# Kernel optimization log

Hardware: AMD Instinct MI355X
Metric: run time of the kernel (lower is better)

The kernel has to match this reference:

```python
import jax, jax.numpy as jnp
import numpy as np


def soft_threshold(x, theta):
    # sign(x) * relu(|x| - theta)
    return jnp.sign(x) * jax.nn.relu(jnp.abs(x) - theta)


def setup_inputs() -> dict:
    key = jax.random.key(0)
    k1, k2, k3, k4 = jax.random.split(key, 4)
    B, n, m = 16384, 256, 1024
    X = jax.random.normal(k1, (B, n), dtype=jnp.float32)
    # xavier-like scaling for weights
    We = jax.random.normal(k2, (m, n), dtype=jnp.float32) * (1.0 / np.sqrt(n))
    S = jax.random.normal(k3, (m, m), dtype=jnp.float32) * (1.0 / np.sqrt(m))
    theta = jax.random.uniform(k4, (m,), dtype=jnp.float32) * 0.1 + 0.05
    return {"X": X, "We": We, "S": S, "theta": theta}


def reference(X, We, S, theta):
    T = 16  # number of unrolled LISTA steps
    B = X @ We.T                      # (batch, m)
    Z0 = soft_threshold(B, theta)

    def step(Z, _):
        C = B + Z @ S.T               # (batch, m)
        Z_new = soft_threshold(C, theta)
        return Z_new, None

    Z, _ = jax.lax.scan(step, Z0, None, length=T)
    return Z
```

## Files before the change

kernel.cpp:

```cpp
#include <hip/hip_runtime.h>
#include <hip/hip_bf16.h>
#include <cstdint>


typedef __attribute__((ext_vector_type(8))) short short8;
typedef __attribute__((ext_vector_type(4))) float floatx4;

__device__ __forceinline__ void g2lds16(const void* g, void* lds) {
    __builtin_amdgcn_global_load_lds(
        (const __attribute__((address_space(1))) uint32_t*)(uintptr_t)g,
        (__attribute__((address_space(3))) uint32_t*)(uintptr_t)lds,
        16, 0, 0);
}

template<int KSTEPS, bool FIRST, bool LAST>
__global__ void __launch_bounds__(256, 3)
lista_gemm(const unsigned short* __restrict__ A,
           const unsigned short* __restrict__ W,
           const float* __restrict__ Bmat_in,
           float* __restrict__ Bmat_out,
           const float* __restrict__ theta,
           unsigned short* __restrict__ Zout,
           float* __restrict__ Fout)
{
    constexpr int K  = KSTEPS * 64;
    constexpr int N  = 1024;
    constexpr int KB = K * 2;

    __shared__ unsigned short Ash[128 * 64];
    __shared__ unsigned short Bsh[128 * 64];

    const int t    = threadIdx.x;
    const int bm   = blockIdx.x;
    const int bn   = blockIdx.y;
    const int wave = t >> 6;
    const int lane = t & 63;
    const int wm   = wave >> 1;
    const int wn   = wave & 1;

    floatx4 acc[4][4];
#pragma unroll
    for (int i = 0; i < 4; ++i)
#pragma unroll
        for (int j = 0; j < 4; ++j) acc[i][j] = (floatx4){0.f, 0.f, 0.f, 0.f};

    const int r0 = t >> 3;
    const int ch = t & 7;

    const char* Abase = (const char*)A + (size_t)(bm * 128) * KB;
    const char* Wbase = (const char*)W + (size_t)(bn * 128) * KB;

    for (int kt = 0; kt < KSTEPS; ++kt) {
        __syncthreads();
#pragma unroll
        for (int c = 0; c < 4; ++c) {
            const int r = r0 + c * 32;
            const int g = ch ^ (r & 7);
            const size_t goff = (size_t)r * KB + (size_t)kt * 128 + g * 16;
            const int loff = (c * 256 + t) * 16;
            g2lds16(Abase + goff, (char*)Ash + loff);
            g2lds16(Wbase + goff, (char*)Bsh + loff);
        }
        __syncthreads();

#pragma unroll
        for (int kk = 0; kk < 2; ++kk) {
            short8 af[4], bf[4];
            const int q  = lane >> 4;
            const int rl = lane & 15;
            const int gq = kk * 4 + q;
#pragma unroll
            for (int mi = 0; mi < 4; ++mi) {
                const int R = wm * 64 + mi * 16 + rl;
                af[mi] = *(const short8*)((const char*)Ash + R * 128 + ((gq ^ (R & 7)) * 16));
            }
#pragma unroll
            for (int ni = 0; ni < 4; ++ni) {
                const int R = wn * 64 + ni * 16 + rl;
                bf[ni] = *(const short8*)((const char*)Bsh + R * 128 + ((gq ^ (R & 7)) * 16));
            }
#pragma unroll
            for (int mi = 0; mi < 4; ++mi)
#pragma unroll
                for (int ni = 0; ni < 4; ++ni)
                    acc[mi][ni] = __builtin_amdgcn_mfma_f32_16x16x32_bf16(
                        af[mi], bf[ni], acc[mi][ni], 0, 0, 0);
        }
    }

    const int col_base = bn * 128 + wn * 64;
    const int row_base = bm * 128 + wm * 64;
#pragma unroll
    for (int ni = 0; ni < 4; ++ni) {
        const int col = col_base + ni * 16 + (lane & 15);
        const float th = theta[col];
#pragma unroll
        for (int mi = 0; mi < 4; ++mi) {
            const int row0 = row_base + mi * 16 + (lane >> 4) * 4;
#pragma unroll
            for (int v = 0; v < 4; ++v) {
                const size_t idx = (size_t)(row0 + v) * N + col;
                float c = acc[mi][ni][v];
                if constexpr (!FIRST) c += Bmat_in[idx];
                if constexpr (FIRST)  Bmat_out[idx] = c;
                const float a = fabsf(c) - th;
                const float z = a > 0.f ? (c > 0.f ? a : -a) : 0.f;
                if constexpr (LAST) {
                    Fout[idx] = z;
                } else {
                    __hip_bfloat16 hb = __float2bfloat16(z);
                    Zout[idx] = *(unsigned short*)&hb;
                }
            }
        }
    }
}

__global__ void __launch_bounds__(256)
cvt4(const float* __restrict__ s, unsigned short* __restrict__ d, int n4)
{
    const int i = blockIdx.x * blockDim.x + threadIdx.x;
    if (i < n4) {
        const float4 v = ((const float4*)s)[i];
        ushort4 o;
        __hip_bfloat16 b;
        b = __float2bfloat16(v.x); o.x = *(unsigned short*)&b;
        b = __float2bfloat16(v.y); o.y = *(unsigned short*)&b;
        b = __float2bfloat16(v.z); o.z = *(unsigned short*)&b;
        b = __float2bfloat16(v.w); o.w = *(unsigned short*)&b;
        ((ushort4*)d)[i] = o;
    }
}

extern "C" void kernel_launch(void* const* d_in, const int* in_sizes, int n_in,
                              void* d_out, int out_size, void* d_ws, size_t ws_size,
                              hipStream_t stream) {
    const float* X     = (const float*)d_in[0];
    const float* We    = (const float*)d_in[1];
    const float* S     = (const float*)d_in[2];
    const float* theta = (const float*)d_in[3];
    float* out = (float*)d_out;

    char* ws = (char*)d_ws;
    unsigned short* S_bf  = (unsigned short*)(ws);
    unsigned short* X_bf  = (unsigned short*)(ws + (size_t)(2)   * 1048576);
    unsigned short* We_bf = (unsigned short*)(ws + (size_t)(10)  * 1048576);
    float*          Bmat  = (float*)         (ws + (size_t)(11)  * 1048576);
    unsigned short* Za    = (unsigned short*)(ws + (size_t)(75)  * 1048576);
    unsigned short* Zb    = (unsigned short*)(ws + (size_t)(107) * 1048576);

    cvt4<<<dim3(1024), dim3(256), 0, stream>>>(S,  S_bf,  1024 * 1024 / 4);
    cvt4<<<dim3(4096), dim3(256), 0, stream>>>(X,  X_bf,  16384 * 256 / 4);
    cvt4<<<dim3(256),  dim3(256), 0, stream>>>(We, We_bf, 1024 * 256 / 4);

    const dim3 grid(128, 8), blk(256);

    lista_gemm<4, true, false><<<grid, blk, 0, stream>>>(
        X_bf, We_bf, nullptr, Bmat, theta, Za, nullptr);

    unsigned short* zin = Za;
    unsigned short* zout = Zb;
    for (int tstep = 1; tstep <= 15; ++tstep) {
        lista_gemm<16, false, false><<<grid, blk, 0, stream>>>(
            zin, S_bf, Bmat, nullptr, theta, zout, nullptr);
        unsigned short* tmp = zin; zin = zout; zout = tmp;
    }
    lista_gemm<16, false, true><<<grid, blk, 0, stream>>>(
        zin, S_bf, Bmat, nullptr, theta, nullptr, out);
}
```

Measured before the change: 1.048 ms.

## Fuse all LISTA steps into one persistent kernel with Z resident in LDS

Replaces the 17 separate GEMM launches with one kernel in which each 512-thread block owns 64 batch rows. The block keeps its Z tile (64x1024 bf16, 128KB) in swizzled LDS across all 16 steps and keeps B in registers, packed as bf16. This removes the global round-trips of Z and the fp32 B matrix, plus the launch overhead. In exchange, S is streamed directly from global/L2 into registers with no LDS staging. Only 256 blocks run, and B is now stored in bf16 precision, which adds rounding error.

```diff
diff --git a/kernel.cpp b/kernel.cpp
--- a/kernel.cpp
+++ b/kernel.cpp
@@ -6,110 +6,159 @@
 typedef __attribute__((ext_vector_type(8))) short short8;
 typedef __attribute__((ext_vector_type(4))) float floatx4;
 
-__device__ __forceinline__ void g2lds16(const void* g, void* lds) {
-    __builtin_amdgcn_global_load_lds(
-        (const __attribute__((address_space(1))) uint32_t*)(uintptr_t)g,
-        (__attribute__((address_space(3))) uint32_t*)(uintptr_t)lds,
-        16, 0, 0);
+__device__ __forceinline__ unsigned short f2b(float f) {
+    __hip_bfloat16 h = __float2bfloat16(f);
+    return *(unsigned short*)&h;
+}
+__device__ __forceinline__ float b2f(unsigned short u) {
+    union { unsigned int i; float f; } x; x.i = ((unsigned int)u) << 16; return x.f;
 }
 
-template<int KSTEPS, bool FIRST, bool LAST>
-__global__ void __launch_bounds__(256, 3)
-lista_gemm(const unsigned short* __restrict__ A,
-           const unsigned short* __restrict__ W,
-           const float* __restrict__ Bmat_in,
-           float* __restrict__ Bmat_out,
-           const float* __restrict__ theta,
-           unsigned short* __restrict__ Zout,
-           float* __restrict__ Fout)
+__global__ void __launch_bounds__(512, 2)
+lista_fused(const unsigned short* __restrict__ Xbf,
+            const unsigned short* __restrict__ Webf,
+            const unsigned short* __restrict__ Sbf,
+            const float* __restrict__ theta,
+            float* __restrict__ out)
 {
-    constexpr int K  = KSTEPS * 64;
-    constexpr int N  = 1024;
-    constexpr int KB = K * 2;
-
-    __shared__ unsigned short Ash[128 * 64];
-    __shared__ unsigned short Bsh[128 * 64];
+    __shared__ __align__(16) unsigned short Zd[64 * 1024];
 
     const int t    = threadIdx.x;
-    const int bm   = blockIdx.x;
-    const int bn   = blockIdx.y;
     const int wave = t >> 6;
     const int lane = t & 63;
-    const int wm   = wave >> 1;
-    const int wn   = wave & 1;
+    const int l15  = lane & 15;
+    const int q    = lane >> 4;
+    const int blk  = blockIdx.x;
 
-    floatx4 acc[4][4];
+    floatx4 acc[4][8];
+    unsigned int Bpk[4][8][2];
+
+    const char* Sb = (const char*)Sbf  + ((size_t)(wave * 128 + l15) * 1024 + q * 8) * 2;
+    const char* Xb = (const char*)Xbf  + ((size_t)(blk * 64   + l15) * 256  + q * 8) * 2;
+    const char* Wb = (const char*)Webf + ((size_t)(wave * 128 + l15) * 256  + q * 8) * 2;
+
 #pragma unroll
-    for (int i = 0; i < 4; ++i)
+    for (int mi = 0; mi < 4; ++mi)
 #pragma unroll
-        for (int j = 0; j < 4; ++j) acc[i][j] = (floatx4){0.f, 0.f, 0.f, 0.f};
+        for (int ni = 0; ni < 8; ++ni) acc[mi][ni] = (floatx4){0.f, 0.f, 0.f, 0.f};
 
-    const int r0 = t >> 3;
-    const int ch = t & 7;
+#pragma unroll
+    for (int kc = 0; kc < 8; ++kc) {
+        short8 af[4];
+#pragma unroll
+        for (int mi = 0; mi < 4; ++mi)
+            af[mi] = *(const short8*)(Xb + mi * 8192 + kc * 64);
+#pragma unroll
+        for (int h = 0; h < 2; ++h) {
+            short8 sf[4];
+#pragma unroll
+            for (int j = 0; j < 4; ++j)
+                sf[j] = *(const short8*)(Wb + (h * 4 + j) * 8192 + kc * 64);
+#pragma unroll
+            for (int mi = 0; mi < 4; ++mi)
+#pragma unroll
+                for (int j = 0; j < 4; ++j)
+                    acc[mi][h * 4 + j] = __builtin_amdgcn_mfma_f32_16x16x32_bf16(
+                        af[mi], sf[j], acc[mi][h * 4 + j], 0, 0, 0);
+        }
+    }
 
-    const char* Abase = (const char*)A + (size_t)(bm * 128) * KB;
-    const char* Wbase = (const char*)W + (size_t)(bn * 128) * KB;
+#pragma unroll
+    for (int mi = 0; mi < 4; ++mi) {
+#pragma unroll
+        for (int ni = 0; ni < 8; ++ni) {
+            const int col   = wave * 128 + ni * 16 + l15;
+            const float th  = theta[col];
+            const int chunk = col >> 3;
+            const int coff  = (col & 7) * 2;
+#pragma unroll
+            for (int vp = 0; vp < 2; ++vp) {
+                const float c0 = acc[mi][ni][vp * 2 + 0];
+                const float c1 = acc[mi][ni][vp * 2 + 1];
+                const unsigned short b0 = f2b(c0), b1 = f2b(c1);
+                Bpk[mi][ni][vp] = (unsigned int)b0 | ((unsigned int)b1 << 16);
+                const float a0 = fabsf(c0) - th, a1 = fabsf(c1) - th;
+                const float z0 = a0 > 0.f ? copysignf(a0, c0) : 0.f;
+                const float z1 = a1 > 0.f ? copysignf(a1, c1) : 0.f;
+                const int r0 = mi * 16 + q * 4 + vp * 2;
+                const int r1 = r0 + 1;
+                const int s0 = (chunk & ~7) | ((chunk ^ r0) & 7);
+                const int s1 = (chunk & ~7) | ((chunk ^ r1) & 7);
+                *(unsigned short*)((char*)Zd + r0 * 2048 + s0 * 16 + coff) = f2b(z0);
+                *(unsigned short*)((char*)Zd + r1 * 2048 + s1 * 16 + coff) = f2b(z1);
+                acc[mi][ni][vp * 2 + 0] = b2f(b0);
+                acc[mi][ni][vp * 2 + 1] = b2f(b1);
+            }
+        }
+    }
+    __syncthreads();
 
-    for (int kt = 0; kt < KSTEPS; ++kt) {
-        __syncthreads();
+#pragma unroll 1
+    for (int step = 1; step <= 16; ++step) {
+        for (int kc = 0; kc < 32; ++kc) {
+            short8 af[4];
 #pragma unroll
-        for (int c = 0; c < 4; ++c) {
-            const int r = r0 + c * 32;
-            const int g = ch ^ (r & 7);
-            const size_t goff = (size_t)r * KB + (size_t)kt * 128 + g * 16;
-            const int loff = (c * 256 + t) * 16;
-            g2lds16(Abase + goff, (char*)Ash + loff);
-            g2lds16(Wbase + goff, (char*)Bsh + loff);
+            for (int mi = 0; mi < 4; ++mi) {
+                const int row = mi * 16 + l15;
+                const int c   = kc * 4 + q;
+                const int s   = (c & ~7) | ((c ^ row) & 7);
+                af[mi] = *(const short8*)((const char*)Zd + row * 2048 + s * 16);
+            }
+#pragma unroll
+            for (int h = 0; h < 2; ++h) {
+                short8 sf[4];
+#pragma unroll
+                for (int j = 0; j < 4; ++j)
+                    sf[j] = *(const short8*)(Sb + (h * 4 + j) * 32768 + kc * 64);
+#pragma unroll
+                for (int mi = 0; mi < 4; ++mi)
+#pragma unroll
+                    for (int j = 0; j < 4; ++j)
+                        acc[mi][h * 4 + j] = __builtin_amdgcn_mfma_f32_16x16x32_bf16(
+                            af[mi], sf[j], acc[mi][h * 4 + j], 0, 0, 0);
+            }
         }
         __syncthreads();
 
-#pragma unroll
-        for (int kk = 0; kk < 2; ++kk) {
-            short8 af[4], bf[4];
-            const int q  = lane >> 4;
-            const int rl = lane & 15;
-            const int gq = kk * 4 + q;
+        if (step < 16) {
 #pragma unroll
             for (int mi = 0; mi < 4; ++mi) {
-                const int R = wm * 64 + mi * 16 + rl;
-                af[mi] = *(const short8*)((const char*)Ash + R * 128 + ((gq ^ (R & 7)) * 16));
+#pragma unroll
+                for (int ni = 0; ni < 8; ++ni) {
+                    const int col   = wave * 128 + ni * 16 + l15;
+                    const float th  = theta[col];
+                    const int chunk = col >> 3;
+                    const int coff  = (col & 7) * 2;
+#pragma unroll
+                    for (int v = 0; v < 4; ++v) {
+                        const float c = acc[mi][ni][v];
+                        const float a = fabsf(c) - th;
+                        const float z = a > 0.f ? copysignf(a, c) : 0.f;
+                        const int r = mi * 16 + q * 4 + v;
+                        const int s = (chunk & ~7) | ((chunk ^ r) & 7);
+                        *(unsigned short*)((char*)Zd + r * 2048 + s * 16 + coff) = f2b(z);
+                        const unsigned int bp = Bpk[mi][ni][v >> 1];
+                        acc[mi][ni][v] = b2f((v & 1) ? (unsigned short)(bp >> 16)
+                                                     : (unsigned short)(bp & 0xffff));
+                    }
+                }
             }
+            __syncthreads();
+        } else {
 #pragma unroll
-            for (int ni = 0; ni < 4; ++ni) {
-                const int R = wn * 64 + ni * 16 + rl;
-                bf[ni] = *(const short8*)((const char*)Bsh + R * 128 + ((gq ^ (R & 7)) * 16));
-            }
+            for (int mi = 0; mi < 4; ++mi) {
 #pragma unroll
-            for (int mi = 0; mi < 4; ++mi)
+                for (int ni = 0; ni < 8; ++ni) {
+                    const int col  = wave * 128 + ni * 16 + l15;
+                    const float th = theta[col];
 #pragma unroll
-                for (int ni = 0; ni < 4; ++ni)
-                    acc[mi][ni] = __builtin_amdgcn_mfma_f32_16x16x32_bf16(
-                        af[mi], bf[ni], acc[mi][ni], 0, 0, 0);
-        }
-    }
-
-    const int col_base = bn * 128 + wn * 64;
-    const int row_base = bm * 128 + wm * 64;
-#pragma unroll
-    for (int ni = 0; ni < 4; ++ni) {
-        const int col = col_base + ni * 16 + (lane & 15);
-        const float th = theta[col];
-#pragma unroll
-        for (int mi = 0; mi < 4; ++mi) {
-            const int row0 = row_base + mi * 16 + (lane >> 4) * 4;
-#pragma unroll
-            for (int v = 0; v < 4; ++v) {
-                const size_t idx = (size_t)(row0 + v) * N + col;
-                float c = acc[mi][ni][v];
-                if constexpr (!FIRST) c += Bmat_in[idx];
-                if constexpr (FIRST)  Bmat_out[idx] = c;
-                const float a = fabsf(c) - th;
-                const float z = a > 0.f ? (c > 0.f ? a : -a) : 0.f;
-                if constexpr (LAST) {
-                    Fout[idx] = z;
-                } else {
-                    __hip_bfloat16 hb = __float2bfloat16(z);
-                    Zout[idx] = *(unsigned short*)&hb;
+                    for (int v = 0; v < 4; ++v) {
+                        const float c = acc[mi][ni][v];
+                        const float a = fabsf(c) - th;
+                        const float z = a > 0.f ? copysignf(a, c) : 0.f;
+                        const int r = mi * 16 + q * 4 + v;
+                        out[(size_t)(blk * 64 + r) * 1024 + col] = z;
+                    }
                 }
             }
         }
@@ -123,11 +172,7 @@
     if (i < n4) {
         const float4 v = ((const float4*)s)[i];
         ushort4 o;
-        __hip_bfloat16 b;
-        b = __float2bfloat16(v.x); o.x = *(unsigned short*)&b;
-        b = __float2bfloat16(v.y); o.y = *(unsigned short*)&b;
-        b = __float2bfloat16(v.z); o.z = *(unsigned short*)&b;
-        b = __float2bfloat16(v.w); o.w = *(unsigned short*)&b;
+        o.x = f2b(v.x); o.y = f2b(v.y); o.z = f2b(v.z); o.w = f2b(v.w);
         ((ushort4*)d)[i] = o;
     }
 }
@@ -143,28 +188,12 @@
 
     char* ws = (char*)d_ws;
     unsigned short* S_bf  = (unsigned short*)(ws);
-    unsigned short* X_bf  = (unsigned short*)(ws + (size_t)(2)   * 1048576);
-    unsigned short* We_bf = (unsigned short*)(ws + (size_t)(10)  * 1048576);
-    float*          Bmat  = (float*)         (ws + (size_t)(11)  * 1048576);
-    unsigned short* Za    = (unsigned short*)(ws + (size_t)(75)  * 1048576);
-    unsigned short* Zb    = (unsigned short*)(ws + (size_t)(107) * 1048576);
+    unsigned short* X_bf  = (unsigned short*)(ws + (size_t)2  * 1048576);
+    unsigned short* We_bf = (unsigned short*)(ws + (size_t)10 * 1048576);
 
     cvt4<<<dim3(1024), dim3(256), 0, stream>>>(S,  S_bf,  1024 * 1024 / 4);
     cvt4<<<dim3(4096), dim3(256), 0, stream>>>(X,  X_bf,  16384 * 256 / 4);
     cvt4<<<dim3(256),  dim3(256), 0, stream>>>(We, We_bf, 1024 * 256 / 4);
 
-    const dim3 grid(128, 8), blk(256);
-
-    lista_gemm<4, true, false><<<grid, blk, 0, stream>>>(
-        X_bf, We_bf, nullptr, Bmat, theta, Za, nullptr);
-
-    unsigned short* zin = Za;
-    unsigned short* zout = Zb;
-    for (int tstep = 1; tstep <= 15; ++tstep) {
-        lista_gemm<16, false, false><<<grid, blk, 0, stream>>>(
-            zin, S_bf, Bmat, nullptr, theta, zout, nullptr);
-        unsigned short* tmp = zin; zin = zout; zout = tmp;
-    }
-    lista_gemm<16, false, true><<<grid, blk, 0, stream>>>(
-        zin, S_bf, Bmat, nullptr, theta, nullptr, out);
+    lista_fused<<<dim3(256), dim3(512), 0, stream>>>(X_bf, We_bf, S_bf, theta, out);
 }
```

After: 1.653 ms. +57.7%, slower.
